# Kernel tuning notes

Hardware: AMD Instinct MI355X
Metric: run time of the kernel (lower is better)

## Reference

```python
import jax, jax.numpy as jnp
import numpy as np

SMOOTH = 0.5  # self.smooth from __init__

def setup_inputs() -> dict:
    key = jax.random.key(0)
    k1, k2, k3, k4, k5, k6 = jax.random.split(key, 6)
    N, E, F_IN, F_OUT = 100000, 3200000, 128, 128
    x = jax.random.normal(k1, (N, F_IN), dtype=jnp.float32)
    adj_rows = jax.random.randint(k2, (E,), 0, N, dtype=jnp.int32)
    adj_cols = jax.random.randint(k3, (E,), 0, N, dtype=jnp.int32)
    adj_vals = jax.random.uniform(k4, (E,), dtype=jnp.float32)
    stdv = 1.0 / np.sqrt(F_OUT)
    weight = jax.random.uniform(k5, (F_IN, F_OUT), dtype=jnp.float32, minval=-stdv, maxval=stdv)
    bias = jax.random.uniform(k6, (F_OUT,), dtype=jnp.float32, minval=-stdv, maxval=stdv)
    return {"x": x, "adj_rows": adj_rows, "adj_cols": adj_cols,
            "adj_vals": adj_vals, "weight": weight, "bias": bias}

def reference(x, adj_rows, adj_cols, adj_vals, weight, bias):
    # support = X @ W  (dense GEMM)
    support = x @ weight  # [N, F_out]
    n = x.shape[0]
    # adj @ support via edge-list gather + segment scatter-add
    gathered = support[adj_cols] * adj_vals[:, None]  # [E, F_out]
    agg = jax.ops.segment_sum(gathered, adj_rows, num_segments=n)  # [N, F_out]
    # ((I + smooth*adj) / (1 + smooth)) @ support + bias
    out = (support + SMOOTH * agg) / (1.0 + SMOOTH) + bias
    return out
```

## Files before the change

### kernel.cpp

```cpp
#include <hip/hip_runtime.h>
#include <hip/hip_fp16.h>

#define F 128
#define BM 64

#define SB_ROWS 256
#define SB_SHIFT 8
#define NBUCK_MAX 512
#define CAPS 8960
#define KREG 18
#define HBLK 1024
#define NKEY 2048
#define COLG_SHIFT 14

#define LSTR 136

typedef _Float16 half8_t __attribute__((ext_vector_type(8)));
typedef float f32x4 __attribute__((ext_vector_type(4)));

__device__ inline __half2 h2of(unsigned u) {
    union { unsigned u; __half2 h; } x; x.u = u; return x.h;
}

__global__ __launch_bounds__(256) void gemm_kernel(
    const float* __restrict__ X, const float* __restrict__ W,
    _Float16* __restrict__ suph, int N)
{
    __shared__ _Float16 Wt[F * LSTR];
    __shared__ _Float16 Xh[BM * LSTR];

    const int t    = threadIdx.x;
    const int row0 = blockIdx.x * BM;

    for (int i = t; i < F * F; i += 256) {
        int k = i >> 7, c = i & 127;
        Wt[c * LSTR + k] = (_Float16)W[i];
    }
    for (int i = t; i < BM * (F / 4); i += 256) {
        int r = i >> 5, k4 = i & 31;
        int grow = row0 + r;
        float4 xv = make_float4(0.f, 0.f, 0.f, 0.f);
        if (grow < N) xv = ((const float4*)(X + (size_t)grow * F))[k4];
        _Float16* xp = &Xh[r * LSTR + k4 * 4];
        xp[0] = (_Float16)xv.x; xp[1] = (_Float16)xv.y;
        xp[2] = (_Float16)xv.z; xp[3] = (_Float16)xv.w;
    }
    __syncthreads();

    const int wv = t >> 6, lane = t & 63;
    const int fr = lane & 15, fq = lane >> 4;

    const _Float16* xa = Xh + (wv * 16 + fr) * LSTR + fq * 8;
    half8_t a0 = *(const half8_t*)(xa);
    half8_t a1 = *(const half8_t*)(xa + 32);
    half8_t a2 = *(const half8_t*)(xa + 64);
    half8_t a3 = *(const half8_t*)(xa + 96);

    #pragma unroll
    for (int tc = 0; tc < 8; ++tc) {
        const _Float16* wb = Wt + (tc * 16 + fr) * LSTR + fq * 8;
        f32x4 acc = {0.f, 0.f, 0.f, 0.f};
        acc = __builtin_amdgcn_mfma_f32_16x16x32_f16(a0, *(const half8_t*)(wb),      acc, 0, 0, 0);
        acc = __builtin_amdgcn_mfma_f32_16x16x32_f16(a1, *(const half8_t*)(wb + 32), acc, 0, 0, 0);
        acc = __builtin_amdgcn_mfma_f32_16x16x32_f16(a2, *(const half8_t*)(wb + 64), acc, 0, 0, 0);
        acc = __builtin_amdgcn_mfma_f32_16x16x32_f16(a3, *(const half8_t*)(wb + 96), acc, 0, 0, 0);

        const int col   = tc * 16 + fr;
        const int rbase = row0 + wv * 16 + fq * 4;
        #pragma unroll
        for (int r = 0; r < 4; ++r) {
            int row = rbase + r;
            if (row < N) suph[(size_t)row * F + col] = (_Float16)acc[r];
        }
    }
}

__global__ __launch_bounds__(256) void hist_kernel(
    const int* __restrict__ rows, int* __restrict__ counts, int E, int nbuck)
{
    __shared__ int hist[NBUCK_MAX];
    const int t = threadIdx.x;
    int chunk = ((E + HBLK - 1) / HBLK + 3) & ~3;
    const int beg = blockIdx.x * chunk;
    const int end = min(beg + chunk, E);

    for (int b = t; b < nbuck; b += 256) hist[b] = 0;
    __syncthreads();

    if (beg < E) {
        int i = beg + t * 4;
        for (; i + 3 < end; i += 1024) {
            int4 r = *(const int4*)(rows + i);
            atomicAdd(&hist[r.x >> SB_SHIFT], 1);
            atomicAdd(&hist[r.y >> SB_SHIFT], 1);
            atomicAdd(&hist[r.z >> SB_SHIFT], 1);
            atomicAdd(&hist[r.w >> SB_SHIFT], 1);
        }
        for (; i < end; ++i) atomicAdd(&hist[rows[i] >> SB_SHIFT], 1);
    }
    __syncthreads();

    int* my = counts + (size_t)blockIdx.x * nbuck;
    for (int b = t; b < nbuck; b += 256) my[b] = hist[b];
}

__global__ __launch_bounds__(512) void scan_kernel(
    const int* __restrict__ counts, int* __restrict__ bases,
    int* __restrict__ totals, int nbuck)
{
    __shared__ int wsum[8];
    const int b = blockIdx.x;
    const int t = threadIdx.x;
    const int lane = t & 63, w = t >> 6;

    int v0 = counts[(size_t)(2 * t)     * nbuck + b];
    int v1 = counts[(size_t)(2 * t + 1) * nbuck + b];
    int s = v0 + v1;
    int inc = s;
    #pragma unroll
    for (int d = 1; d < 64; d <<= 1) {
        int u = __shfl_up(inc, d, 64);
        if (lane >= d) inc += u;
    }
    if (lane == 63) wsum[w] = inc;
    __syncthreads();
    int wbase = 0;
    #pragma unroll
    for (int ww = 0; ww < 8; ++ww) if (ww < w) wbase += wsum[ww];
    int ex = inc - s + wbase;
    bases[(size_t)(2 * t)     * nbuck + b] = ex;
    bases[(size_t)(2 * t + 1) * nbuck + b] = ex + v0;
    if (t == 0) {
        int tot = 0;
        #pragma unroll
        for (int ww = 0; ww < 8; ++ww) tot += wsum[ww];
        totals[b] = tot;
    }
}

__global__ __launch_bounds__(256) void place_kernel(
    const int* __restrict__ rows, const int* __restrict__ cols,
    const float* __restrict__ vals, const int* __restrict__ bases,
    int2* __restrict__ csr, int E, int nbuck)
{
    __shared__ int base[NBUCK_MAX];
    __shared__ int lc[NBUCK_MAX];

    const int t = threadIdx.x;
    int chunk = ((E + HBLK - 1) / HBLK + 3) & ~3;
    const int beg = blockIdx.x * chunk;
    const int end = min(beg + chunk, E);
    if (beg >= E) return;

    const int* my = bases + (size_t)blockIdx.x * nbuck;
    for (int b = t; b < nbuck; b += 256) { base[b] = my[b]; lc[b] = 0; }
    __syncthreads();

    int i = beg + t * 4;
    for (; i + 3 < end; i += 1024) {
        int4 r = *(const int4*)(rows + i);
        int4 c = *(const int4*)(cols + i);
        float4 v = *(const float4*)(vals + i);
        int rr[4] = {r.x, r.y, r.z, r.w};
        int cc[4] = {c.x, c.y, c.z, c.w};
        float vv[4] = {v.x, v.y, v.z, v.w};
        #pragma unroll
        for (int k = 0; k < 4; ++k) {
            int b  = rr[k] >> SB_SHIFT;
            int rl = rr[k] & (SB_ROWS - 1);
            int pos = base[b] + atomicAdd(&lc[b], 1);
            if (pos < CAPS)
                csr[(size_t)b * CAPS + pos] =
                    make_int2(cc[k] | (rl << 17), __float_as_int(vv[k]));
        }
    }
    for (; i < end; ++i) {
        int b  = rows[i] >> SB_SHIFT;
        int rl = rows[i] & (SB_ROWS - 1);
        int pos = base[b] + atomicAdd(&lc[b], 1);
        if (pos < CAPS)
            csr[(size_t)b * CAPS + pos] =
                make_int2(cols[i] | (rl << 17), __float_as_int(vals[i]));
    }
}

__global__ __launch_bounds__(512) void sortb_kernel(
    const int* __restrict__ totals, int2* __restrict__ csr,
    int* __restrict__ offsB, int* __restrict__ offsE, int N)
{
    __shared__ int sc[NKEY];
    __shared__ int wsum[8];
    __shared__ int2 st[CAPS];

    const int b = blockIdx.x;
    const int t = threadIdx.x;
    const int cnt = min(totals[b], CAPS);
    int2* reg = csr + (size_t)b * CAPS;

    int2 e[KREG];
    #pragma unroll
    for (int k = 0; k < KREG; ++k) {
        int idx = t + k * 512;
        e[k] = (idx < cnt) ? reg[idx] : make_int2(-1, 0);
    }

    for (int i = t; i < NKEY; i += 512) sc[i] = 0;
    __syncthreads();

    #pragma unroll
    for (int k = 0; k < KREG; ++k) {
        if (e[k].x >= 0) {
            unsigned p = (unsigned)e[k].x;
            int key = (int)(((p >> 17) << 3) | ((p >> COLG_SHIFT) & 7));
            atomicAdd(&sc[key], 1);
        }
    }
    __syncthreads();

    int c0 = sc[t * 4], c1 = sc[t * 4 + 1], c2 = sc[t * 4 + 2], c3 = sc[t * 4 + 3];
    int s = c0 + c1 + c2 + c3;
    int inc = s;
    const int lane = t & 63, w = t >> 6;
    #pragma unroll
    for (int d = 1; d < 64; d <<= 1) {
        int u = __shfl_up(inc, d, 64);
        if (lane >= d) inc += u;
    }
    if (lane == 63) wsum[w] = inc;
    __syncthreads();
    int wbase = 0;
    #pragma unroll
    for (int ww = 0; ww < 8; ++ww) if (ww < w) wbase += wsum[ww];
    int run = inc - s + wbase;
    sc[t * 4]     = run; run += c0;
    sc[t * 4 + 1] = run; run += c1;
    sc[t * 4 + 2] = run; run += c2;
    sc[t * 4 + 3] = run; run += c3;
    __syncthreads();

    if (t < SB_ROWS) {
        int row = b * SB_ROWS + t;
        if (row < N) {
            int gbase = b * CAPS;
            int x0 = sc[t * 8];
            int x1 = (t == SB_ROWS - 1) ? cnt : sc[t * 8 + 8];
            offsB[row] = gbase + x0;
            offsE[row] = gbase + x1;
        }
    }
    __syncthreads();

    #pragma unroll
    for (int k = 0; k < KREG; ++k) {
        if (e[k].x >= 0) {
            unsigned p = (unsigned)e[k].x;
            int key = (int)(((p >> 17) << 3) | ((p >> COLG_SHIFT) & 7));
            int pos = atomicAdd(&sc[key], 1);
            st[pos] = make_int2(e[k].x & 0x1FFFF, e[k].y);
        }
    }
    __syncthreads();

    for (int i = t; i < cnt; i += 512) reg[i] = st[i];
}

__global__ __launch_bounds__(256) void agg_kernel(
    const int* __restrict__ offsB, const int* __restrict__ offsE,
    const int2* __restrict__ csr, const __half* __restrict__ sup,
    const float* __restrict__ bias, float* __restrict__ out, int N)
{
    int wid  = (int)((blockIdx.x * 256 + threadIdx.x) >> 6);
    if (wid >= N) return;
    int lane = threadIdx.x & 63;
    int g  = lane >> 4;
    int sl = lane & 15;

    const int beg = offsB[wid];
    const int end = offsE[wid];
    const int len = end - beg;
    const int q   = (len + 3) >> 2;
    const int gb  = beg + g * q;
    const int ge  = min(gb + q, end);

    float acc[8];
    #pragma unroll
    for (int i = 0; i < 8; ++i) acc[i] = 0.f;

    int j = gb;
    for (; j + 3 < ge; j += 4) {
        int2 cv0 = csr[j];
        int2 cv1 = csr[j + 1];
        int2 cv2 = csr[j + 2];
        int2 cv3 = csr[j + 3];
        const uint4 s0 = *(const uint4*)(sup + (size_t)cv0.x * F + sl * 8);
        const uint4 s1 = *(const uint4*)(sup + (size_t)cv1.x * F + sl * 8);
        const uint4 s2 = *(const uint4*)(sup + (size_t)cv2.x * F + sl * 8);
        const uint4 s3 = *(const uint4*)(sup + (size_t)cv3.x * F + sl * 8);
        __half2 v0 = __float2half2_rn(__int_as_float(cv0.y));
        __half2 v1 = __float2half2_rn(__int_as_float(cv1.y));
        __half2 v2 = __float2half2_rn(__int_as_float(cv2.y));
        __half2 v3 = __float2half2_rn(__int_as_float(cv3.y));

        __half2 p0 = __hmul2(h2of(s0.x), v0);
        __half2 p1 = __hmul2(h2of(s0.y), v0);
        __half2 p2 = __hmul2(h2of(s0.z), v0);
        __half2 p3 = __hmul2(h2of(s0.w), v0);
        p0 = __hfma2(h2of(s1.x), v1, p0);
        p1 = __hfma2(h2of(s1.y), v1, p1);
        p2 = __hfma2(h2of(s1.z), v1, p2);
        p3 = __hfma2(h2of(s1.w), v1, p3);
        p0 = __hfma2(h2of(s2.x), v2, p0);
        p1 = __hfma2(h2of(s2.y), v2, p1);
        p2 = __hfma2(h2of(s2.z), v2, p2);
        p3 = __hfma2(h2of(s2.w), v2, p3);
        p0 = __hfma2(h2of(s3.x), v3, p0);
        p1 = __hfma2(h2of(s3.y), v3, p1);
        p2 = __hfma2(h2of(s3.z), v3, p2);
        p3 = __hfma2(h2of(s3.w), v3, p3);

        float2 f;
        f = __half22float2(p0); acc[0] += f.x; acc[1] += f.y;
        f = __half22float2(p1); acc[2] += f.x; acc[3] += f.y;
        f = __half22float2(p2); acc[4] += f.x; acc[5] += f.y;
        f = __half22float2(p3); acc[6] += f.x; acc[7] += f.y;
    }
    for (; j < ge; ++j) {
        int2 cv = csr[j];
        const uint4 s = *(const uint4*)(sup + (size_t)cv.x * F + sl * 8);
        __half2 v = __float2half2_rn(__int_as_float(cv.y));
        float2 f;
        f = __half22float2(__hmul2(h2of(s.x), v)); acc[0] += f.x; acc[1] += f.y;
        f = __half22float2(__hmul2(h2of(s.y), v)); acc[2] += f.x; acc[3] += f.y;
        f = __half22float2(__hmul2(h2of(s.z), v)); acc[4] += f.x; acc[5] += f.y;
        f = __half22float2(__hmul2(h2of(s.w), v)); acc[6] += f.x; acc[7] += f.y;
    }

    #pragma unroll
    for (int i = 0; i < 8; ++i) {
        acc[i] += __shfl_xor(acc[i], 16, 64);
        acc[i] += __shfl_xor(acc[i], 32, 64);
    }

    if (g == 0) {
        const uint4 s = *(const uint4*)(sup + (size_t)wid * F + sl * 8);
        float4 b0 = *(const float4*)(bias + sl * 8);
        float4 b1 = *(const float4*)(bias + sl * 8 + 4);
        const float inv = 1.0f / 1.5f, third = 1.0f / 3.0f;
        float2 sA = __half22float2(h2of(s.x));
        float2 sB = __half22float2(h2of(s.y));
        float2 sC = __half22float2(h2of(s.z));
        float2 sD = __half22float2(h2of(s.w));
        float4 o0, o1;
        o0.x = sA.x * inv + acc[0] * third + b0.x;
        o0.y = sA.y * inv + acc[1] * third + b0.y;
        o0.z = sB.x * inv + acc[2] * third + b0.z;
        o0.w = sB.y * inv + acc[3] * third + b0.w;
        o1.x = sC.x * inv + acc[4] * third + b1.x;
        o1.y = sC.y * inv + acc[5] * third + b1.y;
        o1.z = sD.x * inv + acc[6] * third + b1.z;
        o1.w = sD.y * inv + acc[7] * third + b1.w;
        float* op = out + (size_t)wid * F + sl * 8;
        *(float4*)(op)     = o0;
        *(float4*)(op + 4) = o1;
    }
}

extern "C" void kernel_launch(void* const* d_in, const int* in_sizes, int n_in,
                              void* d_out, int out_size, void* d_ws, size_t ws_size,
                              hipStream_t stream) {
    const float* x        = (const float*)d_in[0];
    const int*   adj_rows = (const int*)  d_in[1];
    const int*   adj_cols = (const int*)  d_in[2];
    const float* adj_vals = (const float*)d_in[3];
    const float* weight   = (const float*)d_in[4];
    const float* bias     = (const float*)d_in[5];

    const int N = in_sizes[0] / F;
    const int E = in_sizes[1];
    const int nbuck = (N + SB_ROWS - 1) / SB_ROWS;

    float* out = (float*)d_out;
    char*  ws  = (char*)d_ws;

    auto align = [](size_t v) { return (v + 255) & ~(size_t)255; };
    size_t off_sup    = 0;
    size_t sz_sup     = align((size_t)N * F * sizeof(_Float16));
    size_t off_csr    = off_sup + sz_sup;
    size_t sz_csr     = align((size_t)nbuck * CAPS * sizeof(int2));
    size_t off_offsB  = off_csr + sz_csr;
    size_t sz_offsB   = align((size_t)N * sizeof(int));
    size_t off_offsE  = off_offsB + sz_offsB;
    size_t sz_offsE   = align((size_t)N * sizeof(int));
    size_t off_counts = off_offsE + sz_offsE;
    size_t sz_counts  = align((size_t)HBLK * nbuck * sizeof(int));
    size_t off_bases  = off_counts + sz_counts;
    size_t sz_bases   = align((size_t)HBLK * nbuck * sizeof(int));
    size_t off_totals = off_bases + sz_bases;

    _Float16* suph = (_Float16*)(ws + off_sup);
    int2* csr    = (int2*)(ws + off_csr);
    int*  offsB  = (int*) (ws + off_offsB);
    int*  offsE  = (int*) (ws + off_offsE);
    int*  counts = (int*) (ws + off_counts);
    int*  bases  = (int*) (ws + off_bases);
    int*  totals = (int*) (ws + off_totals);

    gemm_kernel<<<(N + BM - 1) / BM, 256, 0, stream>>>(x, weight, suph, N);

    hist_kernel<<<HBLK, 256, 0, stream>>>(adj_rows, counts, E, nbuck);

    scan_kernel<<<nbuck, 512, 0, stream>>>(counts, bases, totals, nbuck);

    place_kernel<<<HBLK, 256, 0, stream>>>(
        adj_rows, adj_cols, adj_vals, bases, csr, E, nbuck);

    sortb_kernel<<<nbuck, 512, 0, stream>>>(totals, csr, offsB, offsE, N);

    agg_kernel<<<(N + 3) / 4, 256, 0, stream>>>(
        offsB, offsE, csr, (const __half*)suph, bias, out, N);
}
```

Baseline: 197.9 us.

## Fuse bucket sort with aggregation and stage placement scatter through LDS

```diff
diff --git a/kernel.cpp b/kernel.cpp
--- a/kernel.cpp
+++ b/kernel.cpp
@@ -10,6 +10,7 @@
 #define CAPS 8960
 #define KREG 18
 #define HBLK 1024
+#define PCH 3200
 #define NKEY 2048
 #define COLG_SHIFT 14
 
@@ -143,20 +144,58 @@
     const float* __restrict__ vals, const int* __restrict__ bases,
     int2* __restrict__ csr, int E, int nbuck)
 {
-    __shared__ int base[NBUCK_MAX];
-    __shared__ int lc[NBUCK_MAX];
+    __shared__ int2 st[PCH];
+    __shared__ int  di[PCH];
+    __shared__ int  hist[NBUCK_MAX];
+    __shared__ int  lstart[NBUCK_MAX];
+    __shared__ int  myofs[NBUCK_MAX];
+    __shared__ int  wsum[4];
 
     const int t = threadIdx.x;
     int chunk = ((E + HBLK - 1) / HBLK + 3) & ~3;
     const int beg = blockIdx.x * chunk;
     const int end = min(beg + chunk, E);
     if (beg >= E) return;
+    const int cnt = end - beg;
 
     const int* my = bases + (size_t)blockIdx.x * nbuck;
-    for (int b = t; b < nbuck; b += 256) { base[b] = my[b]; lc[b] = 0; }
+    for (int b = t; b < nbuck; b += 256) { hist[b] = 0; myofs[b] = my[b]; }
     __syncthreads();
 
     int i = beg + t * 4;
+    for (; i + 3 < end; i += 1024) {
+        int4 r = *(const int4*)(rows + i);
+        atomicAdd(&hist[r.x >> SB_SHIFT], 1);
+        atomicAdd(&hist[r.y >> SB_SHIFT], 1);
+        atomicAdd(&hist[r.z >> SB_SHIFT], 1);
+        atomicAdd(&hist[r.w >> SB_SHIFT], 1);
+    }
+    for (; i < end; ++i) atomicAdd(&hist[rows[i] >> SB_SHIFT], 1);
+    __syncthreads();
+
+    {
+        int c0 = hist[2 * t], c1 = hist[2 * t + 1];
+        int s = c0 + c1;
+        int inc = s;
+        const int lane = t & 63, w = t >> 6;
+        #pragma unroll
+        for (int d = 1; d < 64; d <<= 1) {
+            int u = __shfl_up(inc, d, 64);
+            if (lane >= d) inc += u;
+        }
+        if (lane == 63) wsum[w] = inc;
+        __syncthreads();
+        int wbase = 0;
+        #pragma unroll
+        for (int ww = 0; ww < 4; ++ww) if (ww < w) wbase += wsum[ww];
+        int ex = inc - s + wbase;
+        lstart[2 * t]     = ex;
+        lstart[2 * t + 1] = ex + c0;
+        hist[2 * t] = 0; hist[2 * t + 1] = 0;
+    }
+    __syncthreads();
+
+    i = beg + t * 4;
     for (; i + 3 < end; i += 1024) {
         int4 r = *(const int4*)(rows + i);
         int4 c = *(const int4*)(cols + i);
@@ -168,34 +207,48 @@
         for (int k = 0; k < 4; ++k) {
             int b  = rr[k] >> SB_SHIFT;
             int rl = rr[k] & (SB_ROWS - 1);
-            int pos = base[b] + atomicAdd(&lc[b], 1);
-            if (pos < CAPS)
-                csr[(size_t)b * CAPS + pos] =
-                    make_int2(cc[k] | (rl << 17), __float_as_int(vv[k]));
+            int lcv = atomicAdd(&hist[b], 1);
+            int pos = lstart[b] + lcv;
+            if (pos < PCH) {
+                st[pos] = make_int2(cc[k] | (rl << 17), __float_as_int(vv[k]));
+                int o = myofs[b] + lcv;
+                di[pos] = (o < CAPS) ? (b * CAPS + o) : -1;
+            }
         }
     }
     for (; i < end; ++i) {
         int b  = rows[i] >> SB_SHIFT;
         int rl = rows[i] & (SB_ROWS - 1);
-        int pos = base[b] + atomicAdd(&lc[b], 1);
-        if (pos < CAPS)
-            csr[(size_t)b * CAPS + pos] =
-                make_int2(cols[i] | (rl << 17), __float_as_int(vals[i]));
-    }
-}
-
-__global__ __launch_bounds__(512) void sortb_kernel(
-    const int* __restrict__ totals, int2* __restrict__ csr,
-    int* __restrict__ offsB, int* __restrict__ offsE, int N)
+        int lcv = atomicAdd(&hist[b], 1);
+        int pos = lstart[b] + lcv;
+        if (pos < PCH) {
+            st[pos] = make_int2(cols[i] | (rl << 17), __float_as_int(vals[i]));
+            int o = myofs[b] + lcv;
+            di[pos] = (o < CAPS) ? (b * CAPS + o) : -1;
+        }
+    }
+    __syncthreads();
+
+    for (int p = t; p < cnt && p < PCH; p += 256) {
+        int d = di[p];
+        if (d >= 0) csr[d] = st[p];
+    }
+}
+
+__global__ __launch_bounds__(512, 4) void sortagg_kernel(
+    const int* __restrict__ totals, const int2* __restrict__ csr,
+    const __half* __restrict__ sup, const float* __restrict__ bias,
+    float* __restrict__ out, int N)
 {
-    __shared__ int sc[NKEY];
-    __shared__ int wsum[8];
+    __shared__ int  sc[NKEY];
+    __shared__ int  rowoff[SB_ROWS + 1];
+    __shared__ int  wsum[8];
     __shared__ int2 st[CAPS];
 
     const int b = blockIdx.x;
     const int t = threadIdx.x;
     const int cnt = min(totals[b], CAPS);
-    int2* reg = csr + (size_t)b * CAPS;
+    const int2* reg = csr + (size_t)b * CAPS;
 
     int2 e[KREG];
     #pragma unroll
@@ -217,37 +270,31 @@
     }
     __syncthreads();
 
-    int c0 = sc[t * 4], c1 = sc[t * 4 + 1], c2 = sc[t * 4 + 2], c3 = sc[t * 4 + 3];
-    int s = c0 + c1 + c2 + c3;
-    int inc = s;
-    const int lane = t & 63, w = t >> 6;
-    #pragma unroll
-    for (int d = 1; d < 64; d <<= 1) {
-        int u = __shfl_up(inc, d, 64);
-        if (lane >= d) inc += u;
-    }
-    if (lane == 63) wsum[w] = inc;
-    __syncthreads();
-    int wbase = 0;
-    #pragma unroll
-    for (int ww = 0; ww < 8; ++ww) if (ww < w) wbase += wsum[ww];
-    int run = inc - s + wbase;
-    sc[t * 4]     = run; run += c0;
-    sc[t * 4 + 1] = run; run += c1;
-    sc[t * 4 + 2] = run; run += c2;
-    sc[t * 4 + 3] = run; run += c3;
-    __syncthreads();
-
-    if (t < SB_ROWS) {
-        int row = b * SB_ROWS + t;
-        if (row < N) {
-            int gbase = b * CAPS;
-            int x0 = sc[t * 8];
-            int x1 = (t == SB_ROWS - 1) ? cnt : sc[t * 8 + 8];
-            offsB[row] = gbase + x0;
-            offsE[row] = gbase + x1;
-        }
-    }
+    {
+        int c0 = sc[t * 4], c1 = sc[t * 4 + 1], c2 = sc[t * 4 + 2], c3 = sc[t * 4 + 3];
+        int s = c0 + c1 + c2 + c3;
+        int inc = s;
+        const int lane = t & 63, w = t >> 6;
+        #pragma unroll
+        for (int d = 1; d < 64; d <<= 1) {
+            int u = __shfl_up(inc, d, 64);
+            if (lane >= d) inc += u;
+        }
+        if (lane == 63) wsum[w] = inc;
+        __syncthreads();
+        int wbase = 0;
+        #pragma unroll
+        for (int ww = 0; ww < 8; ++ww) if (ww < w) wbase += wsum[ww];
+        int run = inc - s + wbase;
+        sc[t * 4]     = run; run += c0;
+        sc[t * 4 + 1] = run; run += c1;
+        sc[t * 4 + 2] = run; run += c2;
+        sc[t * 4 + 3] = run; run += c3;
+    }
+    __syncthreads();
+
+    if (t < SB_ROWS) rowoff[t] = sc[t * 8];
+    if (t == 0) rowoff[SB_ROWS] = cnt;
     __syncthreads();
 
     #pragma unroll
@@ -261,107 +308,94 @@
     }
     __syncthreads();
 
-    for (int i = t; i < cnt; i += 512) reg[i] = st[i];
-}
-
-__global__ __launch_bounds__(256) void agg_kernel(
-    const int* __restrict__ offsB, const int* __restrict__ offsE,
-    const int2* __restrict__ csr, const __half* __restrict__ sup,
-    const float* __restrict__ bias, float* __restrict__ out, int N)
-{
-    int wid  = (int)((blockIdx.x * 256 + threadIdx.x) >> 6);
-    if (wid >= N) return;
-    int lane = threadIdx.x & 63;
-    int g  = lane >> 4;
-    int sl = lane & 15;
-
-    const int beg = offsB[wid];
-    const int end = offsE[wid];
-    const int len = end - beg;
-    const int q   = (len + 3) >> 2;
-    const int gb  = beg + g * q;
-    const int ge  = min(gb + q, end);
-
-    float acc[8];
-    #pragma unroll
-    for (int i = 0; i < 8; ++i) acc[i] = 0.f;
-
-    int j = gb;
-    for (; j + 3 < ge; j += 4) {
-        int2 cv0 = csr[j];
-        int2 cv1 = csr[j + 1];
-        int2 cv2 = csr[j + 2];
-        int2 cv3 = csr[j + 3];
-        const uint4 s0 = *(const uint4*)(sup + (size_t)cv0.x * F + sl * 8);
-        const uint4 s1 = *(const uint4*)(sup + (size_t)cv1.x * F + sl * 8);
-        const uint4 s2 = *(const uint4*)(sup + (size_t)cv2.x * F + sl * 8);
-        const uint4 s3 = *(const uint4*)(sup + (size_t)cv3.x * F + sl * 8);
-        __half2 v0 = __float2half2_rn(__int_as_float(cv0.y));
-        __half2 v1 = __float2half2_rn(__int_as_float(cv1.y));
-        __half2 v2 = __float2half2_rn(__int_as_float(cv2.y));
-        __half2 v3 = __float2half2_rn(__int_as_float(cv3.y));
-
-        __half2 p0 = __hmul2(h2of(s0.x), v0);
-        __half2 p1 = __hmul2(h2of(s0.y), v0);
-        __half2 p2 = __hmul2(h2of(s0.z), v0);
-        __half2 p3 = __hmul2(h2of(s0.w), v0);
-        p0 = __hfma2(h2of(s1.x), v1, p0);
-        p1 = __hfma2(h2of(s1.y), v1, p1);
-        p2 = __hfma2(h2of(s1.z), v1, p2);
-        p3 = __hfma2(h2of(s1.w), v1, p3);
-        p0 = __hfma2(h2of(s2.x), v2, p0);
-        p1 = __hfma2(h2of(s2.y), v2, p1);
-        p2 = __hfma2(h2of(s2.z), v2, p2);
-        p3 = __hfma2(h2of(s2.w), v2, p3);
-        p0 = __hfma2(h2of(s3.x), v3, p0);
-        p1 = __hfma2(h2of(s3.y), v3, p1);
-        p2 = __hfma2(h2of(s3.z), v3, p2);
-        p3 = __hfma2(h2of(s3.w), v3, p3);
-
-        float2 f;
-        f = __half22float2(p0); acc[0] += f.x; acc[1] += f.y;
-        f = __half22float2(p1); acc[2] += f.x; acc[3] += f.y;
-        f = __half22float2(p2); acc[4] += f.x; acc[5] += f.y;
-        f = __half22float2(p3); acc[6] += f.x; acc[7] += f.y;
-    }
-    for (; j < ge; ++j) {
-        int2 cv = csr[j];
-        const uint4 s = *(const uint4*)(sup + (size_t)cv.x * F + sl * 8);
-        __half2 v = __float2half2_rn(__int_as_float(cv.y));
-        float2 f;
-        f = __half22float2(__hmul2(h2of(s.x), v)); acc[0] += f.x; acc[1] += f.y;
-        f = __half22float2(__hmul2(h2of(s.y), v)); acc[2] += f.x; acc[3] += f.y;
-        f = __half22float2(__hmul2(h2of(s.z), v)); acc[4] += f.x; acc[5] += f.y;
-        f = __half22float2(__hmul2(h2of(s.w), v)); acc[6] += f.x; acc[7] += f.y;
-    }
-
-    #pragma unroll
-    for (int i = 0; i < 8; ++i) {
-        acc[i] += __shfl_xor(acc[i], 16, 64);
-        acc[i] += __shfl_xor(acc[i], 32, 64);
-    }
-
-    if (g == 0) {
-        const uint4 s = *(const uint4*)(sup + (size_t)wid * F + sl * 8);
-        float4 b0 = *(const float4*)(bias + sl * 8);
-        float4 b1 = *(const float4*)(bias + sl * 8 + 4);
-        const float inv = 1.0f / 1.5f, third = 1.0f / 3.0f;
-        float2 sA = __half22float2(h2of(s.x));
-        float2 sB = __half22float2(h2of(s.y));
-        float2 sC = __half22float2(h2of(s.z));
-        float2 sD = __half22float2(h2of(s.w));
-        float4 o0, o1;
-        o0.x = sA.x * inv + acc[0] * third + b0.x;
-        o0.y = sA.y * inv + acc[1] * third + b0.y;
-        o0.z = sB.x * inv + acc[2] * third + b0.z;
-        o0.w = sB.y * inv + acc[3] * third + b0.w;
-        o1.x = sC.x * inv + acc[4] * third + b1.x;
-        o1.y = sC.y * inv + acc[5] * third + b1.y;
-        o1.z = sD.x * inv + acc[6] * third + b1.z;
-        o1.w = sD.y * inv + acc[7] * third + b1.w;
-        float* op = out + (size_t)wid * F + sl * 8;
-        *(float4*)(op)     = o0;
-        *(float4*)(op + 4) = o1;
+    const int w = t >> 6, lane = t & 63;
+    const int g = lane >> 4, sl = lane & 15;
+    const float inv = 1.0f / 1.5f, third = 1.0f / 3.0f;
+
+    for (int r = w * 32; r < w * 32 + 32; ++r) {
+        int grow = b * SB_ROWS + r;
+        if (grow >= N) break;
+        const int beg = rowoff[r];
+        const int end = rowoff[r + 1];
+        const int len = end - beg;
+        const int q   = (len + 3) >> 2;
+        const int gb  = beg + g * q;
+        const int ge  = min(gb + q, end);
+
+        float acc[8];
+        #pragma unroll
+        for (int i = 0; i < 8; ++i) acc[i] = 0.f;
+
+        int j = gb;
+        for (; j + 7 < ge; j += 8) {
+            int2 cv[8];
+            #pragma unroll
+            for (int k = 0; k < 8; ++k) cv[k] = st[j + k];
+            uint4 ss[8];
+            #pragma unroll
+            for (int k = 0; k < 8; ++k)
+                ss[k] = *(const uint4*)(sup + (size_t)cv[k].x * F + sl * 8);
+
+            __half2 p0, p1, p2, p3;
+            #pragma unroll
+            for (int k = 0; k < 8; ++k) {
+                __half2 v = __float2half2_rn(__int_as_float(cv[k].y));
+                if (k == 0) {
+                    p0 = __hmul2(h2of(ss[0].x), v);
+                    p1 = __hmul2(h2of(ss[0].y), v);
+                    p2 = __hmul2(h2of(ss[0].z), v);
+                    p3 = __hmul2(h2of(ss[0].w), v);
+                } else {
+                    p0 = __hfma2(h2of(ss[k].x), v, p0);
+                    p1 = __hfma2(h2of(ss[k].y), v, p1);
+                    p2 = __hfma2(h2of(ss[k].z), v, p2);
+                    p3 = __hfma2(h2of(ss[k].w), v, p3);
+                }
+            }
+            float2 f;
+            f = __half22float2(p0); acc[0] += f.x; acc[1] += f.y;
+            f = __half22float2(p1); acc[2] += f.x; acc[3] += f.y;
+            f = __half22float2(p2); acc[4] += f.x; acc[5] += f.y;
+            f = __half22float2(p3); acc[6] += f.x; acc[7] += f.y;
+        }
+        for (; j < ge; ++j) {
+            int2 cv = st[j];
+            const uint4 s = *(const uint4*)(sup + (size_t)cv.x * F + sl * 8);
+            __half2 v = __float2half2_rn(__int_as_float(cv.y));
+            float2 f;
+            f = __half22float2(__hmul2(h2of(s.x), v)); acc[0] += f.x; acc[1] += f.y;
+            f = __half22float2(__hmul2(h2of(s.y), v)); acc[2] += f.x; acc[3] += f.y;
+            f = __half22float2(__hmul2(h2of(s.z), v)); acc[4] += f.x; acc[5] += f.y;
+            f = __half22float2(__hmul2(h2of(s.w), v)); acc[6] += f.x; acc[7] += f.y;
+        }
+
+        #pragma unroll
+        for (int i = 0; i < 8; ++i) {
+            acc[i] += __shfl_xor(acc[i], 16, 64);
+            acc[i] += __shfl_xor(acc[i], 32, 64);
+        }
+
+        if (g == 0) {
+            const uint4 s = *(const uint4*)(sup + (size_t)grow * F + sl * 8);
+            float4 b0 = *(const float4*)(bias + sl * 8);
+            float4 b1 = *(const float4*)(bias + sl * 8 + 4);
+            float2 sA = __half22float2(h2of(s.x));
+            float2 sB = __half22float2(h2of(s.y));
+            float2 sC = __half22float2(h2of(s.z));
+            float2 sD = __half22float2(h2of(s.w));
+            float4 o0, o1;
+            o0.x = sA.x * inv + acc[0] * third + b0.x;
+            o0.y = sA.y * inv + acc[1] * third + b0.y;
+            o0.z = sB.x * inv + acc[2] * third + b0.z;
+            o0.w = sB.y * inv + acc[3] * third + b0.w;
+            o1.x = sC.x * inv + acc[4] * third + b1.x;
+            o1.y = sC.y * inv + acc[5] * third + b1.y;
+            o1.z = sD.x * inv + acc[6] * third + b1.z;
+            o1.w = sD.y * inv + acc[7] * third + b1.w;
+            float* op = out + (size_t)grow * F + sl * 8;
+            *(float4*)(op)     = o0;
+            *(float4*)(op + 4) = o1;
+        }
     }
 }
 
@@ -387,11 +421,7 @@
     size_t sz_sup     = align((size_t)N * F * sizeof(_Float16));
     size_t off_csr    = off_sup + sz_sup;
     size_t sz_csr     = align((size_t)nbuck * CAPS * sizeof(int2));
-    size_t off_offsB  = off_csr + sz_csr;
-    size_t sz_offsB   = align((size_t)N * sizeof(int));
-    size_t off_offsE  = off_offsB + sz_offsB;
-    size_t sz_offsE   = align((size_t)N * sizeof(int));
-    size_t off_counts = off_offsE + sz_offsE;
+    size_t off_counts = off_csr + sz_csr;
     size_t sz_counts  = align((size_t)HBLK * nbuck * sizeof(int));
     size_t off_bases  = off_counts + sz_counts;
     size_t sz_bases   = align((size_t)HBLK * nbuck * sizeof(int));
@@ -399,8 +429,6 @@
 
     _Float16* suph = (_Float16*)(ws + off_sup);
     int2* csr    = (int2*)(ws + off_csr);
-    int*  offsB  = (int*) (ws + off_offsB);
-    int*  offsE  = (int*) (ws + off_offsE);
     int*  counts = (int*) (ws + off_counts);
     int*  bases  = (int*) (ws + off_bases);
     int*  totals = (int*) (ws + off_totals);
@@ -414,8 +442,6 @@
     place_kernel<<<HBLK, 256, 0, stream>>>(
         adj_rows, adj_cols, adj_vals, bases, csr, E, nbuck);
 
-    sortb_kernel<<<nbuck, 512, 0, stream>>>(totals, csr, offsB, offsE, N);
-
-    agg_kernel<<<(N + 3) / 4, 256, 0, stream>>>(
-        offsB, offsE, csr, (const __half*)suph, bias, out, N);
-}
+    sortagg_kernel<<<nbuck, 512, 0, stream>>>(
+        totals, csr, (const __half*)suph, bias, out, N);
+}
```

Measured after the change: 198.0 us. No clear change (+0.0%).

## Stage bucket scatter in LDS and use nontemporal loads/stores in SpMM

Applied to the files above, without the earlier changes.

```diff
diff --git a/kernel.cpp b/kernel.cpp
--- a/kernel.cpp
+++ b/kernel.cpp
@@ -10,6 +10,7 @@
 #define CAPS 8960
 #define KREG 18
 #define HBLK 1024
+#define PCH 3200
 #define NKEY 2048
 #define COLG_SHIFT 14
 
@@ -20,6 +21,15 @@
 
 __device__ inline __half2 h2of(unsigned u) {
     union { unsigned u; __half2 h; } x; x.u = u; return x.h;
+}
+__device__ inline int2 ntload_int2(const int2* p) {
+    unsigned long long v = __builtin_nontemporal_load((const unsigned long long*)p);
+    int2 r; r.x = (int)(unsigned)(v & 0xffffffffull); r.y = (int)(unsigned)(v >> 32);
+    return r;
+}
+__device__ inline void ntstore_f4(float* p, float a, float b, float c, float d) {
+    f32x4 v = {a, b, c, d};
+    __builtin_nontemporal_store(v, (f32x4*)p);
 }
 
 __global__ __launch_bounds__(256) void gemm_kernel(
@@ -143,20 +153,58 @@
     const float* __restrict__ vals, const int* __restrict__ bases,
     int2* __restrict__ csr, int E, int nbuck)
 {
-    __shared__ int base[NBUCK_MAX];
-    __shared__ int lc[NBUCK_MAX];
+    __shared__ int2 st[PCH];
+    __shared__ int  di[PCH];
+    __shared__ int  hist[NBUCK_MAX];
+    __shared__ int  lstart[NBUCK_MAX];
+    __shared__ int  myofs[NBUCK_MAX];
+    __shared__ int  wsum[4];
 
     const int t = threadIdx.x;
     int chunk = ((E + HBLK - 1) / HBLK + 3) & ~3;
     const int beg = blockIdx.x * chunk;
     const int end = min(beg + chunk, E);
     if (beg >= E) return;
+    const int cnt = end - beg;
 
     const int* my = bases + (size_t)blockIdx.x * nbuck;
-    for (int b = t; b < nbuck; b += 256) { base[b] = my[b]; lc[b] = 0; }
+    for (int b = t; b < nbuck; b += 256) { hist[b] = 0; myofs[b] = my[b]; }
     __syncthreads();
 
     int i = beg + t * 4;
+    for (; i + 3 < end; i += 1024) {
+        int4 r = *(const int4*)(rows + i);
+        atomicAdd(&hist[r.x >> SB_SHIFT], 1);
+        atomicAdd(&hist[r.y >> SB_SHIFT], 1);
+        atomicAdd(&hist[r.z >> SB_SHIFT], 1);
+        atomicAdd(&hist[r.w >> SB_SHIFT], 1);
+    }
+    for (; i < end; ++i) atomicAdd(&hist[rows[i] >> SB_SHIFT], 1);
+    __syncthreads();
+
+    {
+        int c0 = hist[2 * t], c1 = hist[2 * t + 1];
+        int s = c0 + c1;
+        int inc = s;
+        const int lane = t & 63, w = t >> 6;
+        #pragma unroll
+        for (int d = 1; d < 64; d <<= 1) {
+            int u = __shfl_up(inc, d, 64);
+            if (lane >= d) inc += u;
+        }
+        if (lane == 63) wsum[w] = inc;
+        __syncthreads();
+        int wbase = 0;
+        #pragma unroll
+        for (int ww = 0; ww < 4; ++ww) if (ww < w) wbase += wsum[ww];
+        int ex = inc - s + wbase;
+        lstart[2 * t]     = ex;
+        lstart[2 * t + 1] = ex + c0;
+        hist[2 * t] = 0; hist[2 * t + 1] = 0;
+    }
+    __syncthreads();
+
+    i = beg + t * 4;
     for (; i + 3 < end; i += 1024) {
         int4 r = *(const int4*)(rows + i);
         int4 c = *(const int4*)(cols + i);
@@ -168,19 +216,31 @@
         for (int k = 0; k < 4; ++k) {
             int b  = rr[k] >> SB_SHIFT;
             int rl = rr[k] & (SB_ROWS - 1);
-            int pos = base[b] + atomicAdd(&lc[b], 1);
-            if (pos < CAPS)
-                csr[(size_t)b * CAPS + pos] =
-                    make_int2(cc[k] | (rl << 17), __float_as_int(vv[k]));
+            int lcv = atomicAdd(&hist[b], 1);
+            int pos = lstart[b] + lcv;
+            if (pos < PCH) {
+                st[pos] = make_int2(cc[k] | (rl << 17), __float_as_int(vv[k]));
+                int o = myofs[b] + lcv;
+                di[pos] = (o < CAPS) ? (b * CAPS + o) : -1;
+            }
         }
     }
     for (; i < end; ++i) {
         int b  = rows[i] >> SB_SHIFT;
         int rl = rows[i] & (SB_ROWS - 1);
-        int pos = base[b] + atomicAdd(&lc[b], 1);
-        if (pos < CAPS)
-            csr[(size_t)b * CAPS + pos] =
-                make_int2(cols[i] | (rl << 17), __float_as_int(vals[i]));
+        int lcv = atomicAdd(&hist[b], 1);
+        int pos = lstart[b] + lcv;
+        if (pos < PCH) {
+            st[pos] = make_int2(cols[i] | (rl << 17), __float_as_int(vals[i]));
+            int o = myofs[b] + lcv;
+            di[pos] = (o < CAPS) ? (b * CAPS + o) : -1;
+        }
+    }
+    __syncthreads();
+
+    for (int p = t; p < cnt && p < PCH; p += 256) {
+        int d = di[p];
+        if (d >= 0) csr[d] = st[p];
     }
 }
 
@@ -288,10 +348,10 @@
 
     int j = gb;
     for (; j + 3 < ge; j += 4) {
-        int2 cv0 = csr[j];
-        int2 cv1 = csr[j + 1];
-        int2 cv2 = csr[j + 2];
-        int2 cv3 = csr[j + 3];
+        int2 cv0 = ntload_int2(csr + j);
+        int2 cv1 = ntload_int2(csr + j + 1);
+        int2 cv2 = ntload_int2(csr + j + 2);
+        int2 cv3 = ntload_int2(csr + j + 3);
         const uint4 s0 = *(const uint4*)(sup + (size_t)cv0.x * F + sl * 8);
         const uint4 s1 = *(const uint4*)(sup + (size_t)cv1.x * F + sl * 8);
         const uint4 s2 = *(const uint4*)(sup + (size_t)cv2.x * F + sl * 8);
@@ -325,7 +385,7 @@
         f = __half22float2(p3); acc[6] += f.x; acc[7] += f.y;
     }
     for (; j < ge; ++j) {
-        int2 cv = csr[j];
+        int2 cv = ntload_int2(csr + j);
         const uint4 s = *(const uint4*)(sup + (size_t)cv.x * F + sl * 8);
         __half2 v = __float2half2_rn(__int_as_float(cv.y));
         float2 f;
@@ -350,18 +410,17 @@
         float2 sB = __half22float2(h2of(s.y));
         float2 sC = __half22float2(h2of(s.z));
         float2 sD = __half22float2(h2of(s.w));
-        float4 o0, o1;
-        o0.x = sA.x * inv + acc[0] * third + b0.x;
-        o0.y = sA.y * inv + acc[1] * third + b0.y;
-        o0.z = sB.x * inv + acc[2] * third + b0.z;
-        o0.w = sB.y * inv + acc[3] * third + b0.w;
-        o1.x = sC.x * inv + acc[4] * third + b1.x;
-        o1.y = sC.y * inv + acc[5] * third + b1.y;
-        o1.z = sD.x * inv + acc[6] * third + b1.z;
-        o1.w = sD.y * inv + acc[7] * third + b1.w;
         float* op = out + (size_t)wid * F + sl * 8;
-        *(float4*)(op)     = o0;
-        *(float4*)(op + 4) = o1;
+        ntstore_f4(op,
+                   sA.x * inv + acc[0] * third + b0.x,
+                   sA.y * inv + acc[1] * third + b0.y,
+                   sB.x * inv + acc[2] * third + b0.z,
+                   sB.y * inv + acc[3] * third + b0.w);
+        ntstore_f4(op + 4,
+                   sC.x * inv + acc[4] * third + b1.x,
+                   sC.y * inv + acc[5] * third + b1.y,
+                   sD.x * inv + acc[6] * third + b1.z,
+                   sD.y * inv + acc[7] * third + b1.w);
     }
 }
 
```

Measured after the change: 198.9 us. About the same (+0.5%).
